# Optimization experiments

Hardware: AMD Instinct MI355X
Metric: run time of the kernel (lower is better)

Reference implementation:

```python
import jax, jax.numpy as jnp
from jax import lax
import numpy as np

LRELU_SLOPE = 0.1
DILATIONS = (1, 2, 4)
B, C, T = 8, 256, 8192


def pd_indexing(x, d, dilation):
    """Pitch-dependent past/future gather along time.
    x: (B, C, T); d: (B, 1, T) float dilation factors.
    Returns xP, xF: (B, C, T), zero where index is out of range.
    """
    b, c, t_len = x.shape
    t = jnp.arange(t_len, dtype=x.dtype)  # (T,)
    dil = d[:, 0, :] * dilation           # (B, T)
    idxP = jnp.round(t[None, :] - dil).astype(jnp.int32)  # (B, T)
    idxF = jnp.round(t[None, :] + dil).astype(jnp.int32)  # (B, T)
    validP = (idxP >= 0).astype(x.dtype)[:, None, :]        # (B,1,T)
    validF = (idxF < t_len).astype(x.dtype)[:, None, :]
    idxPc = jnp.broadcast_to(jnp.clip(idxP, 0, t_len - 1)[:, None, :], (b, c, t_len))
    idxFc = jnp.broadcast_to(jnp.clip(idxF, 0, t_len - 1)[:, None, :], (b, c, t_len))
    xP = jnp.take_along_axis(x, idxPc, axis=2) * validP
    xF = jnp.take_along_axis(x, idxFc, axis=2) * validF
    return xP, xF


def conv1x1(x, w, bias):
    # x: (B,C,T), w: (O,C), bias: (O,)
    return jnp.einsum('oc,bct->bot', w, x) + bias[None, :, None]


def conv3(x, w, bias):
    # x: (B,C,T), w: (O,C,3), padding=1
    y = lax.conv_general_dilated(x, w, window_strides=(1,), padding=[(1, 1)],
                                 dimension_numbers=('NCH', 'OIH', 'NCH'))
    return y + bias[None, :, None]


def setup_inputs() -> dict:
    key = jax.random.key(0)
    ks = jax.random.split(key, 8)
    x = jax.random.normal(ks[0], (B, C, T), dtype=jnp.float32)
    d = jax.random.uniform(ks[1], (B, 1, T), dtype=jnp.float32, minval=0.0, maxval=16.0)
    n = len(DILATIONS)
    s1 = 1.0 / np.sqrt(C)
    s3 = 1.0 / np.sqrt(3 * C)
    WC = jax.random.normal(ks[2], (n, C, C), dtype=jnp.float32) * s1
    WP = jax.random.normal(ks[3], (n, C, C), dtype=jnp.float32) * s1
    WF = jax.random.normal(ks[4], (n, C, C), dtype=jnp.float32) * s1
    WA = jax.random.normal(ks[5], (n, C, C, 3), dtype=jnp.float32) * s3
    bC = jnp.zeros((n, C), dtype=jnp.float32)
    bP = jnp.zeros((n, C), dtype=jnp.float32)
    bF = jnp.zeros((n, C), dtype=jnp.float32)
    bA = jnp.zeros((n, C), dtype=jnp.float32)
    return {"x": x, "d": d, "WC": WC, "bC": bC, "WP": WP, "bP": bP,
            "WF": WF, "bF": bF, "WA": WA, "bA": bA}


def reference(x, d, WC, bC, WP, bP, WF, bF, WA, bA):
    for i, dilation in enumerate(DILATIONS):
        xt = jax.nn.leaky_relu(x, LRELU_SLOPE)
        xP, xF = pd_indexing(xt, d, dilation)
        xt = conv1x1(xt, WC[i], bC[i]) + conv1x1(xP, WP[i], bP[i]) + conv1x1(xF, WF[i], bF[i])
        xt = jax.nn.leaky_relu(xt, LRELU_SLOPE)
        xt = conv3(xt, WA[i], bA[i])
        x = xt + x
    return x
```

## Files before the change

### kernel.cpp

```cpp
#include <hip/hip_runtime.h>
#include <hip/hip_bf16.h>
#include <cstddef>
#include <cstdint>

constexpr int Bn = 8, Cn = 256, Tn = 8192;
constexpr int NL = 3;
constexpr int Kc = 768;
constexpr float SLOPE = 0.1f;

typedef unsigned short u16;
using bf8   = __attribute__((ext_vector_type(8))) short;
using f32x4 = __attribute__((ext_vector_type(4))) float;

__device__ __forceinline__ float lrelu(float v) { return v > 0.f ? v : SLOPE * v; }
__device__ __forceinline__ u16 f2bf(float f) {
    __hip_bfloat16 h = __float2bfloat16(f);
    return *reinterpret_cast<u16*>(&h);
}

__device__ __forceinline__ void g2l16(const u16* g, u16* l) {
    __builtin_amdgcn_global_load_lds(
        (const __attribute__((address_space(1))) char*)g,
        (__attribute__((address_space(3))) char*)l, 16, 0, 0);
}

__global__ __launch_bounds__(256)
void k_wprep(const float* __restrict__ WC, const float* __restrict__ WP,
             const float* __restrict__ WF, const float* __restrict__ WA,
             const float* __restrict__ bC, const float* __restrict__ bP,
             const float* __restrict__ bF,
             u16* __restrict__ Wcat, u16* __restrict__ WAp, float* __restrict__ bSum,
             u16* __restrict__ zrow)
{
    if (blockIdx.x == 0) zrow[threadIdx.x] = 0;
    const int n1 = NL * Cn * Kc;
    for (int i = blockIdx.x * blockDim.x + threadIdx.x; i < n1;
         i += gridDim.x * blockDim.x) {
        int c = i % Cn;
        int s = (i / Cn) % 3;
        int o = (i / (3 * Cn)) % Cn;
        int l = i / (3 * Cn * Cn);
        size_t src = ((size_t)l * Cn + o) * Cn + c;
        float wc = (s == 0) ? WC[src] : (s == 1) ? WP[src] : WF[src];
        Wcat[i] = f2bf(wc);
        WAp[i] = f2bf(WA[src * 3 + s]);
    }
    for (int i = blockIdx.x * blockDim.x + threadIdx.x; i < NL * Cn;
         i += gridDim.x * blockDim.x)
        bSum[i] = bC[i] + bP[i] + bF[i];
}

__global__ __launch_bounds__(256)
void k_prep(const float* __restrict__ x, u16* __restrict__ xT)
{
    __shared__ float s[64][65];
    const int b = blockIdx.z, c0 = blockIdx.y * 64, t0 = blockIdx.x * 64;
    const int tid = threadIdx.x;
    const float* xb = x + ((size_t)b * Cn + c0) * Tn + t0;

    int tt = tid & 63, c4 = tid >> 6;
    for (int cc = c4; cc < 64; cc += 4)
        s[cc][tt] = xb[(size_t)cc * Tn + tt];
    __syncthreads();

    int ccS = tid & 63, t4 = tid >> 6;
    u16* xTb = xT + ((size_t)b * Tn + t0) * Cn + c0;
    for (int t2 = t4; t2 < 64; t2 += 4)
        xTb[(size_t)t2 * Cn + ccS] = f2bf(lrelu(s[ccS][t2]));
}

__global__ __launch_bounds__(256)
void k_gemm1(const u16* __restrict__ xT, const float* __restrict__ d,
             const u16* __restrict__ Wl, const float* __restrict__ bS,
             float dil, u16* __restrict__ zT, const u16* __restrict__ zrow)
{
    __shared__ u16 smem[4 * 4096];
    __shared__ int sRow[3][128];

    const int tid = threadIdx.x;
    const int b = blockIdx.z;
    const int t0 = blockIdx.x * 128;
    const int o0 = blockIdx.y * 128;

    if (tid < 128) {
        int t = t0 + tid;
        float dv = d[(size_t)b * Tn + t] * dil;
        int ip = (int)rintf((float)t - dv);
        int iF = (int)rintf((float)t + dv);
        sRow[0][tid] = t;
        sRow[1][tid] = (ip >= 0) ? ip : -1;
        sRow[2][tid] = (iF < Tn) ? iF : -1;
    }
    __syncthreads();

    const int srow = tid >> 2;
    const int schunk = (tid & 3) * 8;
    const u16* xTb = xT + (size_t)b * Tn * Cn;

    const u16 *pr0[3], *pr1[3];
    #pragma unroll
    for (int s = 0; s < 3; ++s) {
        int r0 = sRow[s][srow], r1 = sRow[s][srow + 64];
        pr0[s] = (r0 >= 0) ? (xTb + (size_t)r0 * Cn + schunk) : (zrow + schunk);
        pr1[s] = (r1 >= 0) ? (xTb + (size_t)r1 * Cn + schunk) : (zrow + schunk);
    }
    const u16* wbase = Wl + (size_t)(o0 + srow) * Kc + schunk;

    const int lane = tid & 63, wv = tid >> 6;
    const int wm = (wv & 1) * 64;
    const int wn = (wv >> 1) * 64;
    const int lr = lane & 15, quad = lane >> 4;

    const int ldsW = srow * 32 + schunk;
    const int ldsW2 = (srow + 64) * 32 + schunk;

    auto dma = [&](int kg, int bsel) {
        int seg = kg >> 3, kk = (kg & 7) * 32;
        u16* bx = smem + bsel * 4096;
        u16* bw = smem + 8192 + bsel * 4096;
        g2l16(wbase + seg * 256 + kk,                 bw + ldsW);
        g2l16(wbase + (size_t)64 * Kc + seg * 256 + kk, bw + ldsW2);
        g2l16(pr0[seg] + kk, bx + ldsW);
        g2l16(pr1[seg] + kk, bx + ldsW2);
    };

    f32x4 acc[4][4] = {};
    dma(0, 0);

    #pragma unroll
    for (int kg = 0; kg < 24; ++kg) {
        __syncthreads();
        if (kg + 1 < 24) dma(kg + 1, (kg + 1) & 1);
        const u16* bX = smem + (kg & 1) * 4096;
        const u16* bW = smem + 8192 + (kg & 1) * 4096;

        bf8 af[4], bg[4];
        #pragma unroll
        for (int mi = 0; mi < 4; ++mi)
            af[mi] = *(const bf8*)(bX + (wm + mi * 16 + lr) * 32 + quad * 8);
        #pragma unroll
        for (int ni = 0; ni < 4; ++ni)
            bg[ni] = *(const bf8*)(bW + (wn + ni * 16 + lr) * 32 + quad * 8);
        #pragma unroll
        for (int mi = 0; mi < 4; ++mi)
            #pragma unroll
            for (int ni = 0; ni < 4; ++ni)
                acc[mi][ni] = __builtin_amdgcn_mfma_f32_16x16x32_bf16(
                    af[mi], bg[ni], acc[mi][ni], 0, 0, 0);
    }

    float bias[4];
    #pragma unroll
    for (int ni = 0; ni < 4; ++ni) bias[ni] = bS[o0 + wn + ni * 16 + lr];
    u16* zTb = zT + (size_t)b * Tn * Cn;
    #pragma unroll
    for (int mi = 0; mi < 4; ++mi)
        #pragma unroll
        for (int r = 0; r < 4; ++r) {
            int t = t0 + wm + mi * 16 + quad * 4 + r;
            u16* row = zTb + (size_t)t * Cn + o0 + wn;
            #pragma unroll
            for (int ni = 0; ni < 4; ++ni)
                row[ni * 16 + lr] = f2bf(lrelu(acc[mi][ni][r] + bias[ni]));
        }
}

__global__ __launch_bounds__(256)
void k_gemm2(const u16* __restrict__ zT, const u16* __restrict__ WAl,
             const float* __restrict__ bA, const float* __restrict__ xres,
             float* __restrict__ out, u16* __restrict__ xTn, int writeXT,
             const u16* __restrict__ zrow)
{
    __shared__ u16 smem[4 * 4096];

    const int tid = threadIdx.x;
    const int b = blockIdx.z;
    const int t0 = blockIdx.x * 128;
    const int o0 = blockIdx.y * 128;

    const int srow = tid >> 2;
    const int schunk = (tid & 3) * 8;
    const int lane = tid & 63, wv = tid >> 6;
    const int wo = (wv & 1) * 64;
    const int wt = (wv >> 1) * 64;
    const int lr = lane & 15, quad = lane >> 4;

    const u16* zTb = zT + (size_t)b * Tn * Cn;
    const u16 *zr0[3], *zr1[3];
    #pragma unroll
    for (int tap = 0; tap < 3; ++tap) {
        int r0 = t0 + srow + tap - 1;
        int r1 = r0 + 64;
        zr0[tap] = (r0 >= 0 && r0 < Tn) ? (zTb + (size_t)r0 * Cn + schunk)
                                        : (zrow + schunk);
        zr1[tap] = (r1 >= 0 && r1 < Tn) ? (zTb + (size_t)r1 * Cn + schunk)
                                        : (zrow + schunk);
    }
    const u16* wbase = WAl + (size_t)(o0 + srow) * Kc + schunk;

    const int ldsW = srow * 32 + schunk;
    const int ldsW2 = (srow + 64) * 32 + schunk;

    auto dma = [&](int kg, int bsel) {
        int tap = kg >> 3, kk = (kg & 7) * 32;
        u16* bz = smem + bsel * 4096;
        u16* bw = smem + 8192 + bsel * 4096;
        g2l16(wbase + tap * 256 + kk,                   bw + ldsW);
        g2l16(wbase + (size_t)64 * Kc + tap * 256 + kk, bw + ldsW2);
        g2l16(zr0[tap] + kk, bz + ldsW);
        g2l16(zr1[tap] + kk, bz + ldsW2);
    };

    f32x4 acc[4][4] = {};
    dma(0, 0);

    #pragma unroll
    for (int kg = 0; kg < 24; ++kg) {
        __syncthreads();
        if (kg + 1 < 24) dma(kg + 1, (kg + 1) & 1);
        const u16* bZ = smem + (kg & 1) * 4096;
        const u16* bW = smem + 8192 + (kg & 1) * 4096;

        bf8 af[4], bg[4];
        #pragma unroll
        for (int mi = 0; mi < 4; ++mi)
            af[mi] = *(const bf8*)(bW + (wo + mi * 16 + lr) * 32 + quad * 8);
        #pragma unroll
        for (int ni = 0; ni < 4; ++ni)
            bg[ni] = *(const bf8*)(bZ + (wt + ni * 16 + lr) * 32 + quad * 8);
        #pragma unroll
        for (int mi = 0; mi < 4; ++mi)
            #pragma unroll
            for (int ni = 0; ni < 4; ++ni)
                acc[mi][ni] = __builtin_amdgcn_mfma_f32_16x16x32_bf16(
                    af[mi], bg[ni], acc[mi][ni], 0, 0, 0);
    }

    float biasv[4][4];
    #pragma unroll
    for (int mi = 0; mi < 4; ++mi) {
        float4 bb = *(const float4*)(bA + o0 + wo + mi * 16 + quad * 4);
        biasv[mi][0] = bb.x; biasv[mi][1] = bb.y; biasv[mi][2] = bb.z; biasv[mi][3] = bb.w;
    }

    if (writeXT) {
        u16* strip = smem + wv * 1152;
        u16* xTb2 = xTn + (size_t)b * Tn * Cn;
        #pragma unroll
        for (int ni = 0; ni < 4; ++ni) {
            __syncthreads();
            #pragma unroll
            for (int mi = 0; mi < 4; ++mi) {
                ushort4 pk;
                #pragma unroll
                for (int r = 0; r < 4; ++r) {
                    int o = o0 + wo + mi * 16 + quad * 4 + r;
                    size_t idx = ((size_t)b * Cn + o) * Tn + t0 + wt + ni * 16 + lr;
                    float v = acc[mi][ni][r] + biasv[mi][r] + xres[idx];
                    out[idx] = v;
                    ((u16*)&pk)[r] = f2bf(lrelu(v));
                }
                *(ushort4*)(strip + lr * 72 + mi * 16 + quad * 4) = pk;
            }
            __syncthreads();
            #pragma unroll
            for (int it = 0; it < 2; ++it) {
                int tt = (lane >> 3) + it * 8;
                uint4 vv = *(const uint4*)(strip + tt * 72 + (lane & 7) * 8);
                *(uint4*)(xTb2 + (size_t)(t0 + wt + ni * 16 + tt) * Cn
                          + o0 + wo + (lane & 7) * 8) = vv;
            }
        }
    } else {
        #pragma unroll
        for (int mi = 0; mi < 4; ++mi)
            #pragma unroll
            for (int r = 0; r < 4; ++r) {
                int o = o0 + wo + mi * 16 + quad * 4 + r;
                size_t base = ((size_t)b * Cn + o) * Tn + t0 + wt;
                #pragma unroll
                for (int ni = 0; ni < 4; ++ni) {
                    size_t idx = base + ni * 16 + lr;
                    out[idx] = acc[mi][ni][r] + biasv[mi][r] + xres[idx];
                }
            }
    }
}

extern "C" void kernel_launch(void* const* d_in, const int* in_sizes, int n_in,
                              void* d_out, int out_size, void* d_ws, size_t ws_size,
                              hipStream_t stream)
{
    const float* x  = (const float*)d_in[0];
    const float* d  = (const float*)d_in[1];
    const float* WC = (const float*)d_in[2];
    const float* bC = (const float*)d_in[3];
    const float* WP = (const float*)d_in[4];
    const float* bP = (const float*)d_in[5];
    const float* WF = (const float*)d_in[6];
    const float* bF = (const float*)d_in[7];
    const float* WA = (const float*)d_in[8];
    const float* bA = (const float*)d_in[9];
    float* out = (float*)d_out;

    char* ws = (char*)d_ws;
    u16*   xT   = (u16*)(ws);
    u16*   zT   = (u16*)(ws + (size_t)Bn * Tn * Cn * 2);
    u16*   Wcat = (u16*)(ws + (size_t)2 * Bn * Tn * Cn * 2);
    u16*   WAp  = Wcat + (size_t)NL * Cn * Kc;
    float* bSum = (float*)(WAp + (size_t)NL * Cn * Kc);
    u16*   zrow = (u16*)(bSum + NL * Cn);

    k_wprep<<<dim3(1024), dim3(256), 0, stream>>>(WC, WP, WF, WA, bC, bP, bF,
                                                  Wcat, WAp, bSum, zrow);

    dim3 gP(Tn / 64, Cn / 64, Bn);
    dim3 gG(Tn / 128, Cn / 128, Bn);
    dim3 blk(256);

    k_prep<<<gP, blk, 0, stream>>>(x, xT);

    const float dils[NL] = {1.f, 2.f, 4.f};
    const float* xcur = x;
    for (int i = 0; i < NL; ++i) {
        k_gemm1<<<gG, blk, 0, stream>>>(xT, d,
                                        Wcat + (size_t)i * Cn * Kc,
                                        bSum + (size_t)i * Cn,
                                        dils[i], zT, zrow);
        k_gemm2<<<gG, blk, 0, stream>>>(zT,
                                        WAp + (size_t)i * Cn * Kc,
                                        bA + (size_t)i * Cn,
                                        xcur, out, xT, (i < NL - 1) ? 1 : 0,
                                        zrow);
        xcur = out;
    }
}
```

Measured before the change: 404.8 us.

## Deepen GEMM LDS pipeline to four stages with swizzled layout and priority hints

Both GEMM kernels move from a double-buffered LDS pipeline to a 4-buffer ring with three tiles in flight. The per-step __syncthreads is replaced by explicit vmcnt waits plus a raw barrier, and the next DMA is issued after the fragment reads. An XOR swizzle is applied to the global source chunk and the matching LDS read chunk to cut LDS bank conflicts. MFMA blocks are wrapped in s_setprio to favour math issue. LDS use doubles, which may lower occupancy, and the hand-counted vmcnt values must match the four loads issued per stage.

```diff
diff --git a/kernel.cpp b/kernel.cpp
--- a/kernel.cpp
+++ b/kernel.cpp
@@ -22,6 +22,11 @@
     __builtin_amdgcn_global_load_lds(
         (const __attribute__((address_space(1))) char*)g,
         (__attribute__((address_space(3))) char*)l, 16, 0, 0);
+}
+
+__device__ __forceinline__ void pipe_barrier() {
+    __builtin_amdgcn_s_barrier();
+    __builtin_amdgcn_sched_barrier(0);
 }
 
 __global__ __launch_bounds__(256)
@@ -74,7 +79,7 @@
              const u16* __restrict__ Wl, const float* __restrict__ bS,
              float dil, u16* __restrict__ zT, const u16* __restrict__ zrow)
 {
-    __shared__ u16 smem[4 * 4096];
+    __shared__ u16 smem[8 * 4096];
     __shared__ int sRow[3][128];
 
     const int tid = threadIdx.x;
@@ -94,59 +99,72 @@
     __syncthreads();
 
     const int srow = tid >> 2;
-    const int schunk = (tid & 3) * 8;
+    const int schunkL = (tid & 3) * 8;
+    const int schunkG = ((tid & 3) ^ ((tid >> 3) & 3)) * 8;
     const u16* xTb = xT + (size_t)b * Tn * Cn;
 
     const u16 *pr0[3], *pr1[3];
     #pragma unroll
     for (int s = 0; s < 3; ++s) {
         int r0 = sRow[s][srow], r1 = sRow[s][srow + 64];
-        pr0[s] = (r0 >= 0) ? (xTb + (size_t)r0 * Cn + schunk) : (zrow + schunk);
-        pr1[s] = (r1 >= 0) ? (xTb + (size_t)r1 * Cn + schunk) : (zrow + schunk);
-    }
-    const u16* wbase = Wl + (size_t)(o0 + srow) * Kc + schunk;
+        pr0[s] = (r0 >= 0) ? (xTb + (size_t)r0 * Cn + schunkG) : (zrow + schunkG);
+        pr1[s] = (r1 >= 0) ? (xTb + (size_t)r1 * Cn + schunkG) : (zrow + schunkG);
+    }
+    const u16* wbase = Wl + (size_t)(o0 + srow) * Kc + schunkG;
 
     const int lane = tid & 63, wv = tid >> 6;
     const int wm = (wv & 1) * 64;
     const int wn = (wv >> 1) * 64;
     const int lr = lane & 15, quad = lane >> 4;
-
-    const int ldsW = srow * 32 + schunk;
-    const int ldsW2 = (srow + 64) * 32 + schunk;
+    const int rchunk = (quad ^ ((lr >> 1) & 3)) * 8;
+
+    const int ldsW = srow * 32 + schunkL;
+    const int ldsW2 = (srow + 64) * 32 + schunkL;
 
     auto dma = [&](int kg, int bsel) {
         int seg = kg >> 3, kk = (kg & 7) * 32;
         u16* bx = smem + bsel * 4096;
-        u16* bw = smem + 8192 + bsel * 4096;
-        g2l16(wbase + seg * 256 + kk,                 bw + ldsW);
+        u16* bw = smem + 16384 + bsel * 4096;
+        g2l16(wbase + seg * 256 + kk,                   bw + ldsW);
         g2l16(wbase + (size_t)64 * Kc + seg * 256 + kk, bw + ldsW2);
         g2l16(pr0[seg] + kk, bx + ldsW);
         g2l16(pr1[seg] + kk, bx + ldsW2);
     };
 
     f32x4 acc[4][4] = {};
-    dma(0, 0);
+    dma(0, 0); dma(1, 1); dma(2, 2);
 
     #pragma unroll
     for (int kg = 0; kg < 24; ++kg) {
-        __syncthreads();
-        if (kg + 1 < 24) dma(kg + 1, (kg + 1) & 1);
-        const u16* bX = smem + (kg & 1) * 4096;
-        const u16* bW = smem + 8192 + (kg & 1) * 4096;
+        if (kg < 22)
+            asm volatile("s_waitcnt vmcnt(8) lgkmcnt(0)" ::: "memory");
+        else if (kg == 22)
+            asm volatile("s_waitcnt vmcnt(4) lgkmcnt(0)" ::: "memory");
+        else
+            asm volatile("s_waitcnt vmcnt(0) lgkmcnt(0)" ::: "memory");
+        pipe_barrier();
+
+        const u16* bX = smem + (kg & 3) * 4096;
+        const u16* bW = smem + 16384 + (kg & 3) * 4096;
 
         bf8 af[4], bg[4];
         #pragma unroll
         for (int mi = 0; mi < 4; ++mi)
-            af[mi] = *(const bf8*)(bX + (wm + mi * 16 + lr) * 32 + quad * 8);
+            af[mi] = *(const bf8*)(bX + (wm + mi * 16 + lr) * 32 + rchunk);
         #pragma unroll
         for (int ni = 0; ni < 4; ++ni)
-            bg[ni] = *(const bf8*)(bW + (wn + ni * 16 + lr) * 32 + quad * 8);
+            bg[ni] = *(const bf8*)(bW + (wn + ni * 16 + lr) * 32 + rchunk);
+
+        if (kg + 3 < 24) dma(kg + 3, (kg + 3) & 3);
+
+        __builtin_amdgcn_s_setprio(1);
         #pragma unroll
         for (int mi = 0; mi < 4; ++mi)
             #pragma unroll
             for (int ni = 0; ni < 4; ++ni)
                 acc[mi][ni] = __builtin_amdgcn_mfma_f32_16x16x32_bf16(
                     af[mi], bg[ni], acc[mi][ni], 0, 0, 0);
+        __builtin_amdgcn_s_setprio(0);
     }
 
     float bias[4];
@@ -171,7 +189,7 @@
              float* __restrict__ out, u16* __restrict__ xTn, int writeXT,
              const u16* __restrict__ zrow)
 {
-    __shared__ u16 smem[4 * 4096];
+    __shared__ u16 smem[8 * 4096];
 
     const int tid = threadIdx.x;
     const int b = blockIdx.z;
@@ -179,11 +197,13 @@
     const int o0 = blockIdx.y * 128;
 
     const int srow = tid >> 2;
-    const int schunk = (tid & 3) * 8;
+    const int schunkL = (tid & 3) * 8;
+    const int schunkG = ((tid & 3) ^ ((tid >> 3) & 3)) * 8;
     const int lane = tid & 63, wv = tid >> 6;
     const int wo = (wv & 1) * 64;
     const int wt = (wv >> 1) * 64;
     const int lr = lane & 15, quad = lane >> 4;
+    const int rchunk = (quad ^ ((lr >> 1) & 3)) * 8;
 
     const u16* zTb = zT + (size_t)b * Tn * Cn;
     const u16 *zr0[3], *zr1[3];
@@ -191,20 +211,20 @@
     for (int tap = 0; tap < 3; ++tap) {
         int r0 = t0 + srow + tap - 1;
         int r1 = r0 + 64;
-        zr0[tap] = (r0 >= 0 && r0 < Tn) ? (zTb + (size_t)r0 * Cn + schunk)
-                                        : (zrow + schunk);
-        zr1[tap] = (r1 >= 0 && r1 < Tn) ? (zTb + (size_t)r1 * Cn + schunk)
-                                        : (zrow + schunk);
-    }
-    const u16* wbase = WAl + (size_t)(o0 + srow) * Kc + schunk;
-
-    const int ldsW = srow * 32 + schunk;
-    const int ldsW2 = (srow + 64) * 32 + schunk;
+        zr0[tap] = (r0 >= 0 && r0 < Tn) ? (zTb + (size_t)r0 * Cn + schunkG)
+                                        : (zrow + schunkG);
+        zr1[tap] = (r1 >= 0 && r1 < Tn) ? (zTb + (size_t)r1 * Cn + schunkG)
+                                        : (zrow + schunkG);
+    }
+    const u16* wbase = WAl + (size_t)(o0 + srow) * Kc + schunkG;
+
+    const int ldsW = srow * 32 + schunkL;
+    const int ldsW2 = (srow + 64) * 32 + schunkL;
 
     auto dma = [&](int kg, int bsel) {
         int tap = kg >> 3, kk = (kg & 7) * 32;
         u16* bz = smem + bsel * 4096;
-        u16* bw = smem + 8192 + bsel * 4096;
+        u16* bw = smem + 16384 + bsel * 4096;
         g2l16(wbase + tap * 256 + kk,                   bw + ldsW);
         g2l16(wbase + (size_t)64 * Kc + tap * 256 + kk, bw + ldsW2);
         g2l16(zr0[tap] + kk, bz + ldsW);
@@ -212,28 +232,39 @@
     };
 
     f32x4 acc[4][4] = {};
-    dma(0, 0);
+    dma(0, 0); dma(1, 1); dma(2, 2);
 
     #pragma unroll
     for (int kg = 0; kg < 24; ++kg) {
-        __syncthreads();
-        if (kg + 1 < 24) dma(kg + 1, (kg + 1) & 1);
-        const u16* bZ = smem + (kg & 1) * 4096;
-        const u16* bW = smem + 8192 + (kg & 1) * 4096;
+        if (kg < 22)
+            asm volatile("s_waitcnt vmcnt(8) lgkmcnt(0)" ::: "memory");
+        else if (kg == 22)
+            asm volatile("s_waitcnt vmcnt(4) lgkmcnt(0)" ::: "memory");
+        else
+            asm volatile("s_waitcnt vmcnt(0) lgkmcnt(0)" ::: "memory");
+        pipe_barrier();
+
+        const u16* bZ = smem + (kg & 3) * 4096;
+        const u16* bW = smem + 16384 + (kg & 3) * 4096;
 
         bf8 af[4], bg[4];
         #pragma unroll
         for (int mi = 0; mi < 4; ++mi)
-            af[mi] = *(const bf8*)(bW + (wo + mi * 16 + lr) * 32 + quad * 8);
+            af[mi] = *(const bf8*)(bW + (wo + mi * 16 + lr) * 32 + rchunk);
         #pragma unroll
         for (int ni = 0; ni < 4; ++ni)
-            bg[ni] = *(const bf8*)(bZ + (wt + ni * 16 + lr) * 32 + quad * 8);
+            bg[ni] = *(const bf8*)(bZ + (wt + ni * 16 + lr) * 32 + rchunk);
+
+        if (kg + 3 < 24) dma(kg + 3, (kg + 3) & 3);
+
+        __builtin_amdgcn_s_setprio(1);
         #pragma unroll
         for (int mi = 0; mi < 4; ++mi)
             #pragma unroll
             for (int ni = 0; ni < 4; ++ni)
                 acc[mi][ni] = __builtin_amdgcn_mfma_f32_16x16x32_bf16(
                     af[mi], bg[ni], acc[mi][ni], 0, 0, 0);
+        __builtin_amdgcn_s_setprio(0);
     }
 
     float biasv[4][4];
```

Result: faster. 373.2 us (-7.8%).
